# Kernel tuning notes

Hardware: AMD Instinct MI355X
Metric: run time of the kernel (lower is better)

Reference implementation:

```python
import jax, jax.numpy as jnp
import numpy as np

K = 1024
D = 256
DECAY = 0.99
EPS = 1e-05


def setup_inputs() -> dict:
    key = jax.random.key(0)
    k1, k2 = jax.random.split(key)
    z = jax.random.normal(k1, (16, 4096, D), dtype=jnp.float32)
    codebook = jax.random.normal(k2, (K, D), dtype=jnp.float32)
    cluster_size = jnp.zeros((K,), dtype=jnp.float32)
    embed_avg = jnp.zeros((K, D), dtype=jnp.float32)
    return {"z": z, "codebook": codebook, "cluster_size": cluster_size, "embed_avg": embed_avg}


def reference(z, codebook, cluster_size, embed_avg):
    B, S, d = z.shape
    z_flat = z.reshape(B * S, d)  # (BS, d)
    # L2 distances via ||z||^2 + ||c||^2 - 2 z.c  -> (BS, K)
    z_sq = jnp.sum(z_flat * z_flat, axis=1, keepdims=True)
    c_sq = jnp.sum(codebook * codebook, axis=1)[None, :]
    dist = z_sq + c_sq - 2.0 * (z_flat @ codebook.T)
    indices = jnp.argmin(dist, axis=1)  # (BS,)
    z_q = codebook[indices].reshape(B, S, d)
    # Straight-through estimator
    z_q_st = z + jax.lax.stop_gradient(z_q - z)
    # EMA codebook update (no-grad in original)
    counts = jax.ops.segment_sum(jnp.ones_like(indices, dtype=z.dtype), indices, num_segments=K)
    sums = jax.ops.segment_sum(z_flat, indices, num_segments=K)  # (K, d)
    new_cluster_size = cluster_size * DECAY + counts * (1.0 - DECAY)
    new_embed_avg = embed_avg * DECAY + sums * (1.0 - DECAY)
    new_codebook = new_embed_avg / (new_cluster_size + EPS)[:, None]
    return (z_q_st, indices.reshape(B, S), new_codebook, new_cluster_size, new_embed_avg)
```

## Files before the change

kernel.cpp:

```cpp
#include <hip/hip_runtime.h>

#define N_ROWS 65536
#define DIM    256
#define KCODES 1024

typedef _Float16 h8 __attribute__((ext_vector_type(8)));
typedef _Float16 h4 __attribute__((ext_vector_type(4)));
typedef float    f4 __attribute__((ext_vector_type(4)));

__global__ __launch_bounds__(64) void prep_kernel(const float* __restrict__ cb,
                                                  _Float16* __restrict__ cb_hi,
                                                  _Float16* __restrict__ cb_lo,
                                                  float* __restrict__ csq) {
    const int k = blockIdx.x;
    const int l = threadIdx.x;
    float4 v = reinterpret_cast<const float4*>(cb)[k * 64 + l];
    h4 hv, lv;
    hv[0] = (_Float16)v.x; lv[0] = (_Float16)(v.x - (float)hv[0]);
    hv[1] = (_Float16)v.y; lv[1] = (_Float16)(v.y - (float)hv[1]);
    hv[2] = (_Float16)v.z; lv[2] = (_Float16)(v.z - (float)hv[2]);
    hv[3] = (_Float16)v.w; lv[3] = (_Float16)(v.w - (float)hv[3]);
    *reinterpret_cast<h4*>(&cb_hi[k * 256 + l * 4]) = hv;
    *reinterpret_cast<h4*>(&cb_lo[k * 256 + l * 4]) = lv;
    float s = v.x * v.x + v.y * v.y + v.z * v.z + v.w * v.w;
#pragma unroll
    for (int m = 32; m >= 1; m >>= 1) s += __shfl_xor(s, m, 64);
    if (l == 0) csq[k] = s;
}

__global__ __launch_bounds__(512, 2) void vq_gemm(
    const float* __restrict__ z, const _Float16* __restrict__ cb_hi,
    const _Float16* __restrict__ cb_lo, const float* __restrict__ csq_g,
    float* __restrict__ out_idx, int* __restrict__ idx_ws) {
    __shared__ _Float16 Ahi[128 * 256];
    __shared__ _Float16 Alo[128 * 256];
    __shared__ _Float16 Bhi[128 * 40];
    __shared__ _Float16 Blo[128 * 40];
    __shared__ float red_val[128 * 4];
    __shared__ int   red_idx[128 * 4];

    const int t = threadIdx.x;
    const int row0 = blockIdx.x << 7;
    const int wave = t >> 6;
    const int wr = wave >> 2;
    const int wc = wave & 3;
    const int lane = t & 63;
    const int lm = lane & 15;
    const int lk = lane >> 4;

    {
        const float4* z4 = reinterpret_cast<const float4*>(z) + (size_t)row0 * 64;
#pragma unroll
        for (int i = 0; i < 16; ++i) {
            int f = t + i * 512;
            int row = f >> 6, k4 = f & 63;
            float4 v = z4[f];
            h4 hv, lv;
            hv[0] = (_Float16)v.x; lv[0] = (_Float16)(v.x - (float)hv[0]);
            hv[1] = (_Float16)v.y; lv[1] = (_Float16)(v.y - (float)hv[1]);
            hv[2] = (_Float16)v.z; lv[2] = (_Float16)(v.z - (float)hv[2]);
            hv[3] = (_Float16)v.w; lv[3] = (_Float16)(v.w - (float)hv[3]);
            int idx = (row * 256 + k4 * 4) ^ ((row & 7) << 3);
            *reinterpret_cast<h4*>(&Ahi[idx]) = hv;
            *reinterpret_cast<h4*>(&Alo[idx]) = lv;
        }
    }

    f4 acc[4][2];
    float bval[4][4];
    int   bidx[4][4];
#pragma unroll
    for (int m = 0; m < 4; ++m)
#pragma unroll
        for (int j = 0; j < 4; ++j) { bval[m][j] = 3.4e38f; bidx[m][j] = 0x7fffffff; }

    const f4 zacc = {0.0f, 0.0f, 0.0f, 0.0f};

    for (int ct = 0; ct < 8; ++ct) {
#pragma unroll
        for (int m = 0; m < 4; ++m)
#pragma unroll
            for (int n = 0; n < 2; ++n) acc[m][n] = zacc;

        for (int dc = 0; dc < 8; ++dc) {
            __syncthreads();
            {
                int code = t >> 2, dp = (t & 3) << 3;
                size_t g = (size_t)(ct * 128 + code) * 256 + dc * 32 + dp;
                *reinterpret_cast<h8*>(&Bhi[code * 40 + dp]) =
                    *reinterpret_cast<const h8*>(&cb_hi[g]);
                *reinterpret_cast<h8*>(&Blo[code * 40 + dp]) =
                    *reinterpret_cast<const h8*>(&cb_lo[g]);
            }
            __syncthreads();

            h8 ah[4], al[4], bh[2], bl[2];
#pragma unroll
            for (int m = 0; m < 4; ++m) {
                int row = wr * 64 + m * 16 + lm;
                int idx = (row * 256 + dc * 32 + lk * 8) ^ ((row & 7) << 3);
                ah[m] = *reinterpret_cast<const h8*>(&Ahi[idx]);
                al[m] = *reinterpret_cast<const h8*>(&Alo[idx]);
            }
#pragma unroll
            for (int n = 0; n < 2; ++n) {
                int code = wc * 32 + n * 16 + lm;
                int idx = code * 40 + lk * 8;
                bh[n] = *reinterpret_cast<const h8*>(&Bhi[idx]);
                bl[n] = *reinterpret_cast<const h8*>(&Blo[idx]);
            }
#pragma unroll
            for (int m = 0; m < 4; ++m)
#pragma unroll
                for (int n = 0; n < 2; ++n) {
                    acc[m][n] = __builtin_amdgcn_mfma_f32_16x16x32_f16(ah[m], bh[n], acc[m][n], 0, 0, 0);
                    acc[m][n] = __builtin_amdgcn_mfma_f32_16x16x32_f16(ah[m], bl[n], acc[m][n], 0, 0, 0);
                    acc[m][n] = __builtin_amdgcn_mfma_f32_16x16x32_f16(al[m], bh[n], acc[m][n], 0, 0, 0);
                }
        }

#pragma unroll
        for (int n = 0; n < 2; ++n) {
            int code = ct * 128 + wc * 32 + n * 16 + lm;
            float cs = csq_g[code];
#pragma unroll
            for (int m = 0; m < 4; ++m)
#pragma unroll
                for (int j = 0; j < 4; ++j) {
                    float d = cs - 2.0f * acc[m][n][j];
                    if (d < bval[m][j] || (d == bval[m][j] && code < bidx[m][j])) {
                        bval[m][j] = d;
                        bidx[m][j] = code;
                    }
                }
        }
    }

#pragma unroll
    for (int s = 1; s <= 8; s <<= 1) {
#pragma unroll
        for (int m = 0; m < 4; ++m)
#pragma unroll
            for (int j = 0; j < 4; ++j) {
                float ov = __shfl_xor(bval[m][j], s, 64);
                int   oi = __shfl_xor(bidx[m][j], s, 64);
                if (ov < bval[m][j] || (ov == bval[m][j] && oi < bidx[m][j])) {
                    bval[m][j] = ov;
                    bidx[m][j] = oi;
                }
            }
    }
    if (lm == 0) {
#pragma unroll
        for (int m = 0; m < 4; ++m)
#pragma unroll
            for (int j = 0; j < 4; ++j) {
                int rl = wr * 64 + m * 16 + lk * 4 + j;
                red_val[rl * 4 + wc] = bval[m][j];
                red_idx[rl * 4 + wc] = bidx[m][j];
            }
    }
    __syncthreads();
    if (t < 128) {
        float bv = red_val[t * 4];
        int   bi = red_idx[t * 4];
#pragma unroll
        for (int w = 1; w < 4; ++w) {
            float v = red_val[t * 4 + w];
            int   i2 = red_idx[t * 4 + w];
            if (v < bv || (v == bv && i2 < bi)) { bv = v; bi = i2; }
        }
        out_idx[row0 + t] = (float)bi;
        idx_ws[row0 + t] = bi;
    }
}

__global__ __launch_bounds__(256) void scatter_kernel(
    const float* __restrict__ z, const float* __restrict__ cb,
    const int* __restrict__ idx_ws, float* __restrict__ out_zq,
    float* __restrict__ sums, float* __restrict__ counts) {
    __shared__ int sidx[32];
    const int t = threadIdx.x;
    const int r0 = blockIdx.x << 5;
    if (t < 32) sidx[t] = idx_ws[r0 + t];
    __syncthreads();
#pragma unroll 1
    for (int r = 0; r < 32; ++r) {
        int bk = sidx[r];
        size_t o = (size_t)(r0 + r) * 256 + t;
        float zv = z[o];
        float cv = cb[bk * 256 + t];
        out_zq[o] = zv + (cv - zv);
        atomicAdd(&sums[bk * 256 + t], zv);
    }
    if (t < 32) atomicAdd(&counts[sidx[t]], 1.0f);
}

__global__ __launch_bounds__(256) void ema_kernel(
    const float* __restrict__ cluster_size, const float* __restrict__ embed_avg,
    const float* __restrict__ sums, const float* __restrict__ counts,
    float* __restrict__ out_cb, float* __restrict__ out_cs, float* __restrict__ out_ea) {
    const int k = blockIdx.x, d = threadIdx.x;
    const float DEC = 0.99f;
    const float OM = 1.0f - 0.99f;
    const float EPSV = 1e-5f;
    float ncs = cluster_size[k] * DEC + counts[k] * OM;
    int o = k * 256 + d;
    float nea = embed_avg[o] * DEC + sums[o] * OM;
    out_ea[o] = nea;
    out_cb[o] = nea / (ncs + EPSV);
    if (d == 0) out_cs[k] = ncs;
}

extern "C" void kernel_launch(void* const* d_in, const int* in_sizes, int n_in,
                              void* d_out, int out_size, void* d_ws, size_t ws_size,
                              hipStream_t stream) {
    const float* z            = (const float*)d_in[0];
    const float* cb           = (const float*)d_in[1];
    const float* cluster_size = (const float*)d_in[2];
    const float* embed_avg    = (const float*)d_in[3];

    float* out_zq  = (float*)d_out;
    float* out_idx = out_zq + (size_t)N_ROWS * DIM;
    float* out_cb  = out_idx + N_ROWS;
    float* out_cs  = out_cb + (size_t)KCODES * DIM;
    float* out_ea  = out_cs + KCODES;

    char* w = (char*)d_ws;
    _Float16* cb_hi = (_Float16*)w;                       w += (size_t)KCODES * DIM * 2;
    _Float16* cb_lo = (_Float16*)w;                       w += (size_t)KCODES * DIM * 2;
    float* csq      = (float*)w;                          w += (size_t)KCODES * 4;
    float* sums     = (float*)w;                          w += (size_t)KCODES * DIM * 4;
    float* counts   = (float*)w;                          w += (size_t)KCODES * 4;
    int*   idx_ws   = (int*)w;

    hipMemsetAsync(sums, 0, (size_t)(KCODES * DIM + KCODES) * sizeof(float), stream);
    prep_kernel<<<KCODES, 64, 0, stream>>>(cb, cb_hi, cb_lo, csq);
    vq_gemm<<<N_ROWS / 128, 512, 0, stream>>>(z, cb_hi, cb_lo, csq, out_idx, idx_ws);
    scatter_kernel<<<N_ROWS / 32, 256, 0, stream>>>(z, cb, idx_ws, out_zq, sums, counts);
    ema_kernel<<<KCODES, 256, 0, stream>>>(cluster_size, embed_avg, sums, counts,
                                           out_cb, out_cs, out_ea);
}
```

Measured before the change: 398.2 us.

## Prepack codebook into MFMA fragments and replace atomic scatter with sort-based segment sum

The GEMM now reads pre-packed codebook hi/lo fragments straight from global memory into registers, double-buffered, with no per-chunk LDS staging or barriers. Each wave now covers 64 codes per pass instead of 32, and the code norms are cached in shared memory. The float atomic scatter of sums is replaced by a histogram, a prefix scan, a permutation build and a per-code gather-sum fused with the EMA update. The straight-through output gets its own float4-vectorised kernel. This removes LDS round trips and atomic contention, but adds several small launches and a serial per-code loop whose cost depends on how evenly the codes are used.

```diff
diff --git a/kernel.cpp b/kernel.cpp
--- a/kernel.cpp
+++ b/kernel.cpp
@@ -8,45 +8,59 @@
 typedef _Float16 h4 __attribute__((ext_vector_type(4)));
 typedef float    f4 __attribute__((ext_vector_type(4)));
 
-__global__ __launch_bounds__(64) void prep_kernel(const float* __restrict__ cb,
-                                                  _Float16* __restrict__ cb_hi,
-                                                  _Float16* __restrict__ cb_lo,
-                                                  float* __restrict__ csq) {
+__global__ __launch_bounds__(64) void prep_csq(const float* __restrict__ cb,
+                                               float* __restrict__ csq) {
     const int k = blockIdx.x;
     const int l = threadIdx.x;
     float4 v = reinterpret_cast<const float4*>(cb)[k * 64 + l];
-    h4 hv, lv;
-    hv[0] = (_Float16)v.x; lv[0] = (_Float16)(v.x - (float)hv[0]);
-    hv[1] = (_Float16)v.y; lv[1] = (_Float16)(v.y - (float)hv[1]);
-    hv[2] = (_Float16)v.z; lv[2] = (_Float16)(v.z - (float)hv[2]);
-    hv[3] = (_Float16)v.w; lv[3] = (_Float16)(v.w - (float)hv[3]);
-    *reinterpret_cast<h4*>(&cb_hi[k * 256 + l * 4]) = hv;
-    *reinterpret_cast<h4*>(&cb_lo[k * 256 + l * 4]) = lv;
     float s = v.x * v.x + v.y * v.y + v.z * v.z + v.w * v.w;
 #pragma unroll
     for (int m = 32; m >= 1; m >>= 1) s += __shfl_xor(s, m, 64);
     if (l == 0) csq[k] = s;
 }
 
+__global__ __launch_bounds__(64) void prep_pack(const float* __restrict__ cb,
+                                                _Float16* __restrict__ packB) {
+    const int blk = blockIdx.x;
+    const int G = blk >> 3, dc = blk & 7;
+    const int l = threadIdx.x, lm = l & 15, lk = l >> 4;
+#pragma unroll
+    for (int j = 0; j < 8; ++j) {
+        const int n = j >> 1, h = j & 1;
+        const int code = G * 64 + n * 16 + lm;
+        h8 v;
+#pragma unroll
+        for (int e = 0; e < 8; ++e) {
+            const int d = dc * 32 + lk * 8 + e;
+            float val = cb[code * 256 + d];
+            _Float16 hi = (_Float16)val;
+            v[e] = h ? (_Float16)(val - (float)hi) : hi;
+        }
+        *reinterpret_cast<h8*>(&packB[((blk * 8 + j) << 9) + (l << 3)]) = v;
+    }
+}
+
 __global__ __launch_bounds__(512, 2) void vq_gemm(
-    const float* __restrict__ z, const _Float16* __restrict__ cb_hi,
-    const _Float16* __restrict__ cb_lo, const float* __restrict__ csq_g,
+    const float* __restrict__ z, const _Float16* __restrict__ packB,
+    const float* __restrict__ csq_g,
     float* __restrict__ out_idx, int* __restrict__ idx_ws) {
     __shared__ _Float16 Ahi[128 * 256];
     __shared__ _Float16 Alo[128 * 256];
-    __shared__ _Float16 Bhi[128 * 40];
-    __shared__ _Float16 Blo[128 * 40];
+    __shared__ float csq_s[KCODES];
     __shared__ float red_val[128 * 4];
     __shared__ int   red_idx[128 * 4];
 
     const int t = threadIdx.x;
     const int row0 = blockIdx.x << 7;
     const int wave = t >> 6;
-    const int wr = wave >> 2;
-    const int wc = wave & 3;
+    const int wr  = wave >> 2;
+    const int wcq = wave & 3;
     const int lane = t & 63;
     const int lm = lane & 15;
     const int lk = lane >> 4;
+
+    csq_s[t]       = csq_g[t];
+    csq_s[t + 512] = csq_g[t + 512];
 
     {
         const float4* z4 = reinterpret_cast<const float4*>(z) + (size_t)row0 * 64;
@@ -65,8 +79,8 @@
             *reinterpret_cast<h4*>(&Alo[idx]) = lv;
         }
     }
-
-    f4 acc[4][2];
+    __syncthreads();
+
     float bval[4][4];
     int   bidx[4][4];
 #pragma unroll
@@ -76,25 +90,29 @@
 
     const f4 zacc = {0.0f, 0.0f, 0.0f, 0.0f};
 
-    for (int ct = 0; ct < 8; ++ct) {
+    for (int o = 0; o < 4; ++o) {
+        const int G = o * 4 + wcq;
+        const _Float16* bbase = packB + ((size_t)G << 15);
+
+        f4 acc[4][4];
 #pragma unroll
         for (int m = 0; m < 4; ++m)
 #pragma unroll
-            for (int n = 0; n < 2; ++n) acc[m][n] = zacc;
+            for (int n = 0; n < 4; ++n) acc[m][n] = zacc;
+
+        h8 bcur[8], bnxt[8];
+#pragma unroll
+        for (int j = 0; j < 8; ++j)
+            bcur[j] = *reinterpret_cast<const h8*>(&bbase[(j << 9) + (lane << 3)]);
 
         for (int dc = 0; dc < 8; ++dc) {
-            __syncthreads();
-            {
-                int code = t >> 2, dp = (t & 3) << 3;
-                size_t g = (size_t)(ct * 128 + code) * 256 + dc * 32 + dp;
-                *reinterpret_cast<h8*>(&Bhi[code * 40 + dp]) =
-                    *reinterpret_cast<const h8*>(&cb_hi[g]);
-                *reinterpret_cast<h8*>(&Blo[code * 40 + dp]) =
-                    *reinterpret_cast<const h8*>(&cb_lo[g]);
+            if (dc < 7) {
+                const _Float16* bb = bbase + ((dc + 1) << 12);
+#pragma unroll
+                for (int j = 0; j < 8; ++j)
+                    bnxt[j] = *reinterpret_cast<const h8*>(&bb[(j << 9) + (lane << 3)]);
             }
-            __syncthreads();
-
-            h8 ah[4], al[4], bh[2], bl[2];
+            h8 ah[4], al[4];
 #pragma unroll
             for (int m = 0; m < 4; ++m) {
                 int row = wr * 64 + m * 16 + lm;
@@ -103,26 +121,21 @@
                 al[m] = *reinterpret_cast<const h8*>(&Alo[idx]);
             }
 #pragma unroll
-            for (int n = 0; n < 2; ++n) {
-                int code = wc * 32 + n * 16 + lm;
-                int idx = code * 40 + lk * 8;
-                bh[n] = *reinterpret_cast<const h8*>(&Bhi[idx]);
-                bl[n] = *reinterpret_cast<const h8*>(&Blo[idx]);
-            }
-#pragma unroll
             for (int m = 0; m < 4; ++m)
 #pragma unroll
-                for (int n = 0; n < 2; ++n) {
-                    acc[m][n] = __builtin_amdgcn_mfma_f32_16x16x32_f16(ah[m], bh[n], acc[m][n], 0, 0, 0);
-                    acc[m][n] = __builtin_amdgcn_mfma_f32_16x16x32_f16(ah[m], bl[n], acc[m][n], 0, 0, 0);
-                    acc[m][n] = __builtin_amdgcn_mfma_f32_16x16x32_f16(al[m], bh[n], acc[m][n], 0, 0, 0);
+                for (int n = 0; n < 4; ++n) {
+                    acc[m][n] = __builtin_amdgcn_mfma_f32_16x16x32_f16(ah[m], bcur[n * 2 + 0], acc[m][n], 0, 0, 0);
+                    acc[m][n] = __builtin_amdgcn_mfma_f32_16x16x32_f16(al[m], bcur[n * 2 + 0], acc[m][n], 0, 0, 0);
+                    acc[m][n] = __builtin_amdgcn_mfma_f32_16x16x32_f16(ah[m], bcur[n * 2 + 1], acc[m][n], 0, 0, 0);
                 }
-        }
-
-#pragma unroll
-        for (int n = 0; n < 2; ++n) {
-            int code = ct * 128 + wc * 32 + n * 16 + lm;
-            float cs = csq_g[code];
+#pragma unroll
+            for (int j = 0; j < 8; ++j) bcur[j] = bnxt[j];
+        }
+
+#pragma unroll
+        for (int n = 0; n < 4; ++n) {
+            int code = o * 256 + wcq * 64 + n * 16 + lm;
+            float cs = csq_s[code];
 #pragma unroll
             for (int m = 0; m < 4; ++m)
 #pragma unroll
@@ -156,8 +169,8 @@
 #pragma unroll
             for (int j = 0; j < 4; ++j) {
                 int rl = wr * 64 + m * 16 + lk * 4 + j;
-                red_val[rl * 4 + wc] = bval[m][j];
-                red_idx[rl * 4 + wc] = bidx[m][j];
+                red_val[rl * 4 + wcq] = bval[m][j];
+                red_idx[rl * 4 + wcq] = bidx[m][j];
             }
     }
     __syncthreads();
@@ -175,41 +188,94 @@
     }
 }
 
-__global__ __launch_bounds__(256) void scatter_kernel(
-    const float* __restrict__ z, const float* __restrict__ cb,
-    const int* __restrict__ idx_ws, float* __restrict__ out_zq,
-    float* __restrict__ sums, float* __restrict__ counts) {
+__global__ __launch_bounds__(256) void hist_kernel(const int* __restrict__ idx_ws,
+                                                   int* __restrict__ counts_i) {
+    __shared__ int h[KCODES];
+    const int t = threadIdx.x;
+#pragma unroll
+    for (int i = 0; i < 4; ++i) h[t + i * 256] = 0;
+    __syncthreads();
+    atomicAdd(&h[idx_ws[blockIdx.x * 256 + t]], 1);
+    __syncthreads();
+#pragma unroll
+    for (int i = 0; i < 4; ++i) {
+        int c = h[t + i * 256];
+        if (c) atomicAdd(&counts_i[t + i * 256], c);
+    }
+}
+
+__global__ __launch_bounds__(1024) void scan_kernel(const int* __restrict__ counts_i,
+                                                    int* __restrict__ offsets,
+                                                    int* __restrict__ cursor) {
+    __shared__ int a[KCODES], b[KCODES];
+    const int t = threadIdx.x;
+    int cnt = counts_i[t];
+    a[t] = cnt;
+    __syncthreads();
+    int* src = a; int* dst = b;
+    for (int s = 1; s < 1024; s <<= 1) {
+        dst[t] = (t >= s) ? (src[t - s] + src[t]) : src[t];
+        __syncthreads();
+        int* tmp = src; src = dst; dst = tmp;
+    }
+    int excl = src[t] - cnt;
+    offsets[t] = excl;
+    cursor[t] = excl;
+}
+
+__global__ __launch_bounds__(256) void place_kernel(const int* __restrict__ idx_ws,
+                                                    int* __restrict__ cursor,
+                                                    int* __restrict__ perm) {
+    const int r = blockIdx.x * 256 + threadIdx.x;
+    const int c = idx_ws[r];
+    const int pos = atomicAdd(&cursor[c], 1);
+    perm[pos] = r;
+}
+
+__global__ __launch_bounds__(256) void segsum_ema_kernel(
+    const float* __restrict__ z, const int* __restrict__ perm,
+    const int* __restrict__ offsets, const int* __restrict__ counts_i,
+    const float* __restrict__ cluster_size, const float* __restrict__ embed_avg,
+    float* __restrict__ out_cb, float* __restrict__ out_cs, float* __restrict__ out_ea) {
+    const int k = blockIdx.x, t = threadIdx.x;
+    const int start = offsets[k], n = counts_i[k];
+    float s = 0.0f;
+    for (int i = 0; i < n; ++i) {
+        int r = perm[start + i];
+        s += z[(size_t)r * 256 + t];
+    }
+    const float ncs = cluster_size[k] * 0.99f + (float)n * 0.01f;
+    const int o = k * 256 + t;
+    const float nea = embed_avg[o] * 0.99f + s * 0.01f;
+    out_ea[o] = nea;
+    out_cb[o] = nea / (ncs + 1e-5f);
+    if (t == 0) out_cs[k] = ncs;
+}
+
+__global__ __launch_bounds__(256) void ste_kernel(const float* __restrict__ z,
+                                                  const float* __restrict__ cb,
+                                                  const int* __restrict__ idx_ws,
+                                                  float* __restrict__ out_zq) {
     __shared__ int sidx[32];
     const int t = threadIdx.x;
     const int r0 = blockIdx.x << 5;
     if (t < 32) sidx[t] = idx_ws[r0 + t];
     __syncthreads();
+    const int rs = t >> 6;
+    const int c4 = t & 63;
 #pragma unroll 1
-    for (int r = 0; r < 32; ++r) {
+    for (int it = 0; it < 8; ++it) {
+        int r = it * 4 + rs;
         int bk = sidx[r];
-        size_t o = (size_t)(r0 + r) * 256 + t;
-        float zv = z[o];
-        float cv = cb[bk * 256 + t];
-        out_zq[o] = zv + (cv - zv);
-        atomicAdd(&sums[bk * 256 + t], zv);
-    }
-    if (t < 32) atomicAdd(&counts[sidx[t]], 1.0f);
-}
-
-__global__ __launch_bounds__(256) void ema_kernel(
-    const float* __restrict__ cluster_size, const float* __restrict__ embed_avg,
-    const float* __restrict__ sums, const float* __restrict__ counts,
-    float* __restrict__ out_cb, float* __restrict__ out_cs, float* __restrict__ out_ea) {
-    const int k = blockIdx.x, d = threadIdx.x;
-    const float DEC = 0.99f;
-    const float OM = 1.0f - 0.99f;
-    const float EPSV = 1e-5f;
-    float ncs = cluster_size[k] * DEC + counts[k] * OM;
-    int o = k * 256 + d;
-    float nea = embed_avg[o] * DEC + sums[o] * OM;
-    out_ea[o] = nea;
-    out_cb[o] = nea / (ncs + EPSV);
-    if (d == 0) out_cs[k] = ncs;
+        float4 zv = reinterpret_cast<const float4*>(z)[(size_t)(r0 + r) * 64 + c4];
+        float4 cv = reinterpret_cast<const float4*>(cb)[bk * 64 + c4];
+        float4 ov;
+        ov.x = zv.x + (cv.x - zv.x);
+        ov.y = zv.y + (cv.y - zv.y);
+        ov.z = zv.z + (cv.z - zv.z);
+        ov.w = zv.w + (cv.w - zv.w);
+        reinterpret_cast<float4*>(out_zq)[(size_t)(r0 + r) * 64 + c4] = ov;
+    }
 }
 
 extern "C" void kernel_launch(void* const* d_in, const int* in_sizes, int n_in,
@@ -227,17 +293,23 @@
     float* out_ea  = out_cs + KCODES;
 
     char* w = (char*)d_ws;
-    _Float16* cb_hi = (_Float16*)w;                       w += (size_t)KCODES * DIM * 2;
-    _Float16* cb_lo = (_Float16*)w;                       w += (size_t)KCODES * DIM * 2;
-    float* csq      = (float*)w;                          w += (size_t)KCODES * 4;
-    float* sums     = (float*)w;                          w += (size_t)KCODES * DIM * 4;
-    float* counts   = (float*)w;                          w += (size_t)KCODES * 4;
-    int*   idx_ws   = (int*)w;
-
-    hipMemsetAsync(sums, 0, (size_t)(KCODES * DIM + KCODES) * sizeof(float), stream);
-    prep_kernel<<<KCODES, 64, 0, stream>>>(cb, cb_hi, cb_lo, csq);
-    vq_gemm<<<N_ROWS / 128, 512, 0, stream>>>(z, cb_hi, cb_lo, csq, out_idx, idx_ws);
-    scatter_kernel<<<N_ROWS / 32, 256, 0, stream>>>(z, cb, idx_ws, out_zq, sums, counts);
-    ema_kernel<<<KCODES, 256, 0, stream>>>(cluster_size, embed_avg, sums, counts,
-                                           out_cb, out_cs, out_ea);
-}
+    _Float16* packB = (_Float16*)w;   w += (size_t)KCODES * DIM * 2 * 2;
+    float* csq      = (float*)w;      w += (size_t)KCODES * 4;
+    int* idx_ws     = (int*)w;        w += (size_t)N_ROWS * 4;
+    int* counts_i   = (int*)w;        w += (size_t)KCODES * 4;
+    int* offsets    = (int*)w;        w += (size_t)KCODES * 4;
+    int* cursor     = (int*)w;        w += (size_t)KCODES * 4;
+    int* perm       = (int*)w;
+
+    hipMemsetAsync(counts_i, 0, KCODES * sizeof(int), stream);
+    prep_csq<<<KCODES, 64, 0, stream>>>(cb, csq);
+    prep_pack<<<128, 64, 0, stream>>>(cb, packB);
+    vq_gemm<<<N_ROWS / 128, 512, 0, stream>>>(z, packB, csq, out_idx, idx_ws);
+    hist_kernel<<<N_ROWS / 256, 256, 0, stream>>>(idx_ws, counts_i);
+    scan_kernel<<<1, 1024, 0, stream>>>(counts_i, offsets, cursor);
+    place_kernel<<<N_ROWS / 256, 256, 0, stream>>>(idx_ws, cursor, perm);
+    segsum_ema_kernel<<<KCODES, 256, 0, stream>>>(z, perm, offsets, counts_i,
+                                                  cluster_size, embed_avg,
+                                                  out_cb, out_cs, out_ea);
+    ste_kernel<<<N_ROWS / 32, 256, 0, stream>>>(z, cb, idx_ws, out_zq);
+}
```

New measurement: 1.048 ms. 2.63x slower.
